# Optimization experiments

Hardware: AMD Instinct MI355X
Metric: run time of the kernel (lower is better)

Reference implementation:

```python
import jax, jax.numpy as jnp
import numpy as np

B, T, D, H = 2, 2048, 1024, 16
DH = D // H
EPS = 1e-5


def layer_norm(x, g, b):
    m = jnp.mean(x, axis=-1, keepdims=True)
    v = jnp.mean((x - m) ** 2, axis=-1, keepdims=True)
    return (x - m) * jax.lax.rsqrt(v + EPS) * g + b


def setup_inputs() -> dict:
    key = jax.random.key(0)
    ks = jax.random.split(key, 12)
    s = 0.02
    return {
        "x_refined": jax.random.normal(ks[0], (B, T, D), jnp.float32),
        "x_mem": jax.random.normal(ks[1], (B, T, D), jnp.float32),
        "ln_q_g": jnp.ones((D,), jnp.float32), "ln_q_b": jnp.zeros((D,), jnp.float32),
        "ln_kv_g": jnp.ones((D,), jnp.float32), "ln_kv_b": jnp.zeros((D,), jnp.float32),
        "Wq": jax.random.normal(ks[2], (D, D), jnp.float32) * s,
        "bq": jnp.zeros((D,), jnp.float32),
        "Wk": jax.random.normal(ks[3], (D, D), jnp.float32) * s,
        "bk": jnp.zeros((D,), jnp.float32),
        "Wv": jax.random.normal(ks[4], (D, D), jnp.float32) * s,
        "bv": jnp.zeros((D,), jnp.float32),
        "Wo": jax.random.normal(ks[5], (D, D), jnp.float32) * s,
        "bo": jnp.zeros((D,), jnp.float32),
        "ln_f_g": jnp.ones((D,), jnp.float32), "ln_f_b": jnp.zeros((D,), jnp.float32),
        "W1": jax.random.normal(ks[6], (D, 4 * D), jnp.float32) * s,
        "b1": jnp.zeros((4 * D,), jnp.float32),
        "W2": jax.random.normal(ks[7], (4 * D, D), jnp.float32) * s,
        "b2": jnp.zeros((D,), jnp.float32),
        "band": 24,
    }


def reference(x_refined, x_mem, ln_q_g, ln_q_b, ln_kv_g, ln_kv_b,
              Wq, bq, Wk, bk, Wv, bv, Wo, bo,
              ln_f_g, ln_f_b, W1, b1, W2, b2, band):
    Q = layer_norm(x_refined, ln_q_g, ln_q_b)   # (B,T,D)
    KV = layer_norm(x_mem, ln_kv_g, ln_kv_b)    # (B,T,D)

    # projections, split into heads: (B,H,T,DH)
    q = (Q @ Wq + bq).reshape(B, T, H, DH).transpose(0, 2, 1, 3)
    k = (KV @ Wk + bk).reshape(B, T, H, DH).transpose(0, 2, 1, 3)
    v = (KV @ Wv + bv).reshape(B, T, H, DH).transpose(0, 2, 1, 3)

    scores = jnp.einsum('bhtd,bhsd->bhts', q, k) / jnp.sqrt(jnp.float32(DH))
    # banded additive mask: |t - s| <= band allowed (same math as the Python loop)
    idx = jnp.arange(T)
    allowed = jnp.abs(idx[:, None] - idx[None, :]) <= band  # (T,T)
    scores = jnp.where(allowed[None, None], scores, -jnp.inf)
    attn = jax.nn.softmax(scores, axis=-1)

    ctx = jnp.einsum('bhts,bhsd->bhtd', attn, v)            # (B,H,T,DH)
    ctx = ctx.transpose(0, 2, 1, 3).reshape(B, T, D)
    y = x_refined + (ctx @ Wo + bo)

    h = layer_norm(y, ln_f_g, ln_f_b)
    h = jax.nn.gelu(h @ W1 + b1, approximate=False) @ W2 + b2
    return y + h
```

## Files before the change

kernel.cpp:

```cpp
#include <hip/hip_runtime.h>
#include <math.h>
#include <stdint.h>

#define TSEQ   2048
#define DMODEL 1024
#define NHEAD  16
#define DHEAD  64
#define MROWS  4096

typedef short bf16x8 __attribute__((ext_vector_type(8)));
typedef float f32x4  __attribute__((ext_vector_type(4)));
typedef uint64_t u64x2 __attribute__((ext_vector_type(2)));
typedef unsigned short u16;

typedef __attribute__((address_space(3))) unsigned int lds_u32_t;
typedef __attribute__((address_space(1))) unsigned int glb_u32_t;

static __device__ __forceinline__ u16 f2bf(float f) {
    unsigned u = __float_as_uint(f);
    u += 0x7FFFu + ((u >> 16) & 1u);
    return (u16)(u >> 16);
}
static __device__ __forceinline__ float bf2f(u16 h) {
    return __uint_as_float(((unsigned)h) << 16);
}

__global__ __launch_bounds__(256) void tc_kernel(
    const float* __restrict__ W, u16* __restrict__ Wt, int K, int N)
{
    __shared__ u16 tile[32][33];
    const int n0 = blockIdx.x * 32, k0 = blockIdx.y * 32;
    const int t = threadIdx.x;
    const int tx = t & 31, ty = t >> 5;
#pragma unroll
    for (int i = 0; i < 4; ++i) {
        int kk = ty + i * 8;
        tile[kk][tx] = f2bf(W[(size_t)(k0 + kk) * N + n0 + tx]);
    }
    __syncthreads();
#pragma unroll
    for (int i = 0; i < 4; ++i) {
        int nn = ty + i * 8;
        Wt[(size_t)(n0 + nn) * K + k0 + tx] = tile[tx][nn];
    }
}

__global__ __launch_bounds__(256) void biaspack_kernel(
    const float* __restrict__ bq, const float* __restrict__ bk,
    const float* __restrict__ bv, float* __restrict__ o)
{
    const int i = blockIdx.x * 256 + threadIdx.x;
    if (i < 1024) o[i] = bq[i];
    else if (i < 2048) o[i] = bk[i - 1024];
    else if (i < 3072) o[i] = bv[i - 2048];
}

__global__ __launch_bounds__(256) void vt_kernel(
    const u16* __restrict__ qkv, u16* __restrict__ vT)
{
    __shared__ __align__(16) u16 tile[64][72];
    const int bb = blockIdx.z;
    const int t0 = blockIdx.x * 64;
    const int c0 = blockIdx.y * 64;
    const int tid = threadIdx.x;
    const int r = tid >> 2;
    const int c = (tid & 3) * 16;
    const u16* src = qkv + (size_t)(bb * TSEQ + t0 + r) * 3072 + 2048 + c0 + c;
    *(bf16x8*)&tile[r][c]     = *(const bf16x8*)(src);
    *(bf16x8*)&tile[r][c + 8] = *(const bf16x8*)(src + 8);
    __syncthreads();
    u16 o[16];
#pragma unroll
    for (int j = 0; j < 16; ++j) o[j] = tile[c + j][r];
    u16* dst = vT + (size_t)(bb * 1024 + c0 + r) * TSEQ + t0 + c;
    *(bf16x8*)dst       = *(bf16x8*)&o[0];
    *(bf16x8*)(dst + 8) = *(bf16x8*)&o[8];
}

__global__ __launch_bounds__(256) void ln_kernel(
    const float* __restrict__ x, const float* __restrict__ g,
    const float* __restrict__ b, u16* __restrict__ out)
{
    const int row = blockIdx.x;
    const int t = threadIdx.x;
    const float4 v = ((const float4*)(x + (size_t)row * DMODEL))[t];
    float s  = v.x + v.y + v.z + v.w;
    float s2 = v.x * v.x + v.y * v.y + v.z * v.z + v.w * v.w;
#pragma unroll
    for (int m = 32; m >= 1; m >>= 1) { s += __shfl_xor(s, m); s2 += __shfl_xor(s2, m); }
    __shared__ float ps[4], ps2[4];
    if ((t & 63) == 0) { ps[t >> 6] = s; ps2[t >> 6] = s2; }
    __syncthreads();
    const float S  = ps[0] + ps[1] + ps[2] + ps[3];
    const float S2 = ps2[0] + ps2[1] + ps2[2] + ps2[3];
    const float mean = S * (1.0f / DMODEL);
    const float var  = S2 * (1.0f / DMODEL) - mean * mean;
    const float rstd = rsqrtf(var + 1e-5f);
    const float4 gg = ((const float4*)g)[t];
    const float4 bb = ((const float4*)b)[t];
    u16 o[4];
    o[0] = f2bf((v.x - mean) * rstd * gg.x + bb.x);
    o[1] = f2bf((v.y - mean) * rstd * gg.y + bb.y);
    o[2] = f2bf((v.z - mean) * rstd * gg.z + bb.z);
    o[3] = f2bf((v.w - mean) * rstd * gg.w + bb.w);
    *(short4*)(out + (size_t)row * DMODEL + t * 4) = *(short4*)o;
}

template <int EPI>
__global__ __launch_bounds__(512, 2) void gemm8(
    const u16* __restrict__ A, const u16* __restrict__ A2,
    const u16* __restrict__ Wt, const float* __restrict__ bias,
    u16* __restrict__ Cb, int N, int K, int gx, int cx)
{
    __shared__ __align__(16) char smem8[131072];

    const int bid = blockIdx.x;
    const int xcd = bid & 7, jj = bid >> 3;
    const int sx = gx / cx;
    const int sy = (gridDim.x >> 3) / sx;
    const int xr = xcd / cx, xc = xcd % cx;
    const int jr = jj / sx, jc = jj % sx;
    const int m0 = (xr * sy + jr) * 256;
    const int n0 = (xc * sx + jc) * 256;

    const int tid = threadIdx.x;
    const int lane = tid & 63;
    const int w = tid >> 6;
    const int wr = w >> 2, wc = w & 3;
    const int fr = lane & 15, fq = lane >> 4;
    const int swzoff = (fq ^ ((fr >> 1) & 3)) * 16;

    const u16* Ause = (A2 != nullptr && n0 >= 1024) ? A2 : A;

    const int strow = tid >> 2;
    const int stcol = ((tid & 3) ^ ((tid >> 3) & 3)) * 8;
    const u16* gAs = Ause + (size_t)(m0 + strow) * K + stcol;
    const u16* gBs = Wt  + (size_t)(n0 + strow) * K + stcol;

#define STAGE_A(slot, kt) do {                                                           \
    const u16* _s = gAs + (size_t)(kt) * 32;                                             \
    char* _l = smem8 + (slot) * 32768 + w * 1024;                                        \
    __builtin_amdgcn_global_load_lds((const glb_u32_t*)_s, (lds_u32_t*)_l, 16, 0, 0);    \
    __builtin_amdgcn_global_load_lds((const glb_u32_t*)(_s + (size_t)128 * K),           \
                                     (lds_u32_t*)(_l + 8192), 16, 0, 0);                 \
} while (0)
#define STAGE_B(slot, kt) do {                                                           \
    const u16* _s = gBs + (size_t)(kt) * 32;                                             \
    char* _l = smem8 + (slot) * 32768 + 16384 + w * 1024;                                \
    __builtin_amdgcn_global_load_lds((const glb_u32_t*)_s, (lds_u32_t*)_l, 16, 0, 0);    \
    __builtin_amdgcn_global_load_lds((const glb_u32_t*)(_s + (size_t)128 * K),           \
                                     (lds_u32_t*)(_l + 8192), 16, 0, 0);                 \
} while (0)

    f32x4 zero = {0.f, 0.f, 0.f, 0.f};
    f32x4 acc[8][4];
#pragma unroll
    for (int mi = 0; mi < 8; ++mi)
#pragma unroll
        for (int ni = 0; ni < 4; ++ni) acc[mi][ni] = zero;

    const int nt = K >> 5;
    STAGE_A(0, 0); STAGE_B(0, 0);
    STAGE_A(1, 1); STAGE_B(1, 1);

    const int abase = (wr * 128 + fr) * 64 + swzoff;
    const int bbase = 16384 + (wc * 64 + fr) * 64 + swzoff;

    for (int t = 0; t < nt; ++t) {
        const int slot = t & 3;
        const char* sb = smem8 + slot * 32768;
        asm volatile("s_waitcnt vmcnt(4)" ::: "memory");
        __builtin_amdgcn_s_barrier();

        bf16x8 bfr[4], af[4];
#pragma unroll
        for (int ni = 0; ni < 4; ++ni)
            bfr[ni] = *(const bf16x8*)(sb + bbase + ni * 1024);
#pragma unroll
        for (int mi = 0; mi < 4; ++mi)
            af[mi] = *(const bf16x8*)(sb + abase + mi * 1024);
        if (t + 2 < nt) STAGE_A((t + 2) & 3, t + 2);
        __builtin_amdgcn_s_setprio(1);
#pragma unroll
        for (int mi = 0; mi < 4; ++mi)
#pragma unroll
            for (int ni = 0; ni < 4; ++ni)
                acc[mi][ni] = __builtin_amdgcn_mfma_f32_16x16x32_bf16(af[mi], bfr[ni], acc[mi][ni], 0, 0, 0);
        __builtin_amdgcn_s_setprio(0);

        bf16x8 af2[4];
#pragma unroll
        for (int mi = 0; mi < 4; ++mi)
            af2[mi] = *(const bf16x8*)(sb + abase + (mi + 4) * 1024);
        if (t + 2 < nt) STAGE_B((t + 2) & 3, t + 2);
        __builtin_amdgcn_s_setprio(1);
#pragma unroll
        for (int mi = 0; mi < 4; ++mi)
#pragma unroll
            for (int ni = 0; ni < 4; ++ni)
                acc[mi + 4][ni] = __builtin_amdgcn_mfma_f32_16x16x32_bf16(af2[mi], bfr[ni], acc[mi + 4][ni], 0, 0, 0);
        __builtin_amdgcn_s_setprio(0);
    }
#undef STAGE_A
#undef STAGE_B

    u16* cs = (u16*)smem8;
#pragma unroll
    for (int hh = 0; hh < 2; ++hh) {
        __builtin_amdgcn_s_barrier();
        if (wr == hh) {
#pragma unroll
            for (int ni = 0; ni < 4; ++ni) {
                const int col = wc * 64 + ni * 16 + fr;
                const float bv = bias[n0 + col];
#pragma unroll
                for (int mi = 0; mi < 8; ++mi) {
#pragma unroll
                    for (int j = 0; j < 4; ++j) {
                        float val = acc[mi][ni][j] + bv;
                        if (EPI == 1)
                            val = 0.5f * val * (1.0f + erff(val * 0.70710678118654752f));
                        cs[(mi * 16 + fq * 4 + j) * 260 + col] = f2bf(val);
                    }
                }
            }
        }
        __builtin_amdgcn_s_barrier();
        const int cc = (tid & 31) * 8;
#pragma unroll
        for (int p = 0; p < 8; ++p) {
            const int row = p * 16 + (tid >> 5);
            const uint64_t lo = *(const uint64_t*)&cs[row * 260 + cc];
            const uint64_t hi = *(const uint64_t*)&cs[row * 260 + cc + 4];
            u64x2 v; v.x = lo; v.y = hi;
            *(u64x2*)&Cb[(size_t)(m0 + hh * 128 + row) * N + n0 + cc] = v;
        }
    }
}

template <int EPI>
__global__ __launch_bounds__(256) void gemm_bt(
    const u16* __restrict__ A, const u16* __restrict__ A2,
    const u16* __restrict__ Wt,
    const float* __restrict__ bias, const float* __restrict__ resid,
    u16* __restrict__ Cb, float* __restrict__ Cf, float* __restrict__ Cf2,
    int N, int K, int kl, int gx, int cx)
{
    extern __shared__ __align__(16) char smem[];

    const int bid = blockIdx.x;
    const int xcd = bid & 7, jj = bid >> 3;
    const int sx = gx / cx;
    const int sy = (gridDim.x >> 3) / sx;
    const int xr = xcd / cx, xc = xcd % cx;
    const int jr = jj / sx, jc = jj % sx;
    const int m0 = (xr * sy + jr) * 128;
    const int n0 = (xc * sx + jc) * 128;
    const int kofs = blockIdx.y * kl;

    const int t = threadIdx.x;
    const int lane = t & 63;
    const int wv = t >> 6;
    const int wr = wv >> 1, wc = wv & 1;

    const u16* Ause = (A2 != nullptr && n0 >= 1024) ? A2 : A;

    const int strow = t >> 2;
    const int stcol = (t & 3) * 8;
    const u16* gA  = Ause + (size_t)(m0 + strow) * K + kofs + stcol;
    const u16* gA2 = gA + (size_t)64 * K;
    const u16* gB  = Wt + (size_t)(n0 + strow) * K + kofs + stcol;
    const u16* gB2 = gB + (size_t)64 * K;

#define STAGE(bufi, k0) do {                                                            \
    char* _b = smem + (bufi) * 16384 + wv * 1024;                                       \
    __builtin_amdgcn_global_load_lds((const glb_u32_t*)(gA  + (k0)), (lds_u32_t*)(_b),          16, 0, 0); \
    __builtin_amdgcn_global_load_lds((const glb_u32_t*)(gA2 + (k0)), (lds_u32_t*)(_b + 4096),  16, 0, 0); \
    __builtin_amdgcn_global_load_lds((const glb_u32_t*)(gB  + (k0)), (lds_u32_t*)(_b + 8192),  16, 0, 0); \
    __builtin_amdgcn_global_load_lds((const glb_u32_t*)(gB2 + (k0)), (lds_u32_t*)(_b + 12288), 16, 0, 0); \
} while (0)

    f32x4 zero = {0.f, 0.f, 0.f, 0.f};
    f32x4 acc[4][4];
#pragma unroll
    for (int mi = 0; mi < 4; ++mi)
#pragma unroll
        for (int ni = 0; ni < 4; ++ni) acc[mi][ni] = zero;

    const int fr = lane & 15, fq = lane >> 4;
    const int nk = kl >> 5;

    STAGE(0, 0);
    STAGE(1, 32);

    for (int kt = 0; kt < nk; ++kt) {
        const int cur = kt & 1;
        if (kt < nk - 1) { asm volatile("s_waitcnt vmcnt(4)" ::: "memory"); }
        else             { asm volatile("s_waitcnt vmcnt(0)" ::: "memory"); }
        __builtin_amdgcn_s_barrier();

        const u16* As_ = (const u16*)smem + cur * 8192;
        const u16* Bs_ = As_ + 4096;
        bf16x8 af[4], bfr[4];
#pragma unroll
        for (int mi = 0; mi < 4; ++mi)
            af[mi] = *(const bf16x8*)&As_[(wr * 64 + mi * 16 + fr) * 32 + fq * 8];
#pragma unroll
        for (int ni = 0; ni < 4; ++ni)
            bfr[ni] = *(const bf16x8*)&Bs_[(wc * 64 + ni * 16 + fr) * 32 + fq * 8];

        __builtin_amdgcn_s_setprio(1);
#pragma unroll
        for (int mi = 0; mi < 4; ++mi)
#pragma unroll
            for (int ni = 0; ni < 4; ++ni)
                acc[mi][ni] = __builtin_amdgcn_mfma_f32_16x16x32_bf16(af[mi], bfr[ni], acc[mi][ni], 0, 0, 0);
        __builtin_amdgcn_s_setprio(0);
        __builtin_amdgcn_sched_barrier(0);
        __builtin_amdgcn_s_barrier();
        if (kt + 2 < nk) STAGE(cur, (kt + 2) << 5);
    }
#undef STAGE

    float* Cpart = (EPI == 3) ? (blockIdx.y ? Cf2 : Cf) : Cf;
#pragma unroll
    for (int ni = 0; ni < 4; ++ni) {
        const int col = n0 + wc * 64 + ni * 16 + fr;
        const float bv = (EPI == 3) ? 0.f : bias[col];
#pragma unroll
        for (int mi = 0; mi < 4; ++mi) {
#pragma unroll
            for (int j = 0; j < 4; ++j) {
                const int row = m0 + wr * 64 + mi * 16 + fq * 4 + j;
                float val = acc[mi][ni][j] + bv;
                if (EPI == 2)
                    Cf[(size_t)row * N + col] = val + resid[(size_t)row * N + col];
                else
                    Cpart[(size_t)row * N + col] = val;
            }
        }
    }
}

__global__ __launch_bounds__(256) void redk_kernel(
    const float* __restrict__ p0, const float* __restrict__ p1,
    const float* __restrict__ bias, const float* __restrict__ resid,
    float* __restrict__ out, int n4, int ncols)
{
    const int stride = gridDim.x * 256;
    for (int i = blockIdx.x * 256 + threadIdx.x; i < n4; i += stride) {
        const float4 a = ((const float4*)p0)[i];
        const float4 b = ((const float4*)p1)[i];
        const float4 r = ((const float4*)resid)[i];
        const float4 bb = *(const float4*)&bias[(i * 4) & (ncols - 1)];
        float4 o;
        o.x = a.x + b.x + bb.x + r.x;
        o.y = a.y + b.y + bb.y + r.y;
        o.z = a.z + b.z + bb.z + r.z;
        o.w = a.w + b.w + bb.w + r.w;
        ((float4*)out)[i] = o;
    }
}

__global__ __launch_bounds__(256) void battn_kernel(
    const u16* __restrict__ qkv, const u16* __restrict__ vT,
    u16* __restrict__ ctx, const int* __restrict__ band_ptr)
{
    __shared__ __align__(16) u16 P[4][16][104];
    const int band = *band_ptr;
    const int bid = blockIdx.x;
    const int tile = bid & 31;
    const int h = (bid >> 5) & 15;
    const int b = bid >> 9;
    const int w = threadIdx.x >> 6;
    const int lane = threadIdx.x & 63;
    const int fr = lane & 15, fq = lane >> 4;
    const int t0 = tile * 64 + w * 16;

    const size_t qbase = ((size_t)b * TSEQ) * 3072 + h * DHEAD;
    const size_t kbase = qbase + 1024;
    const size_t cbase = ((size_t)b * TSEQ) * DMODEL + h * DHEAD;

    const bf16x8 aq0 = *(const bf16x8*)&qkv[qbase + (size_t)(t0 + fr) * 3072 + fq * 8];
    const bf16x8 aq1 = *(const bf16x8*)&qkv[qbase + (size_t)(t0 + fr) * 3072 + 32 + fq * 8];

    const int kb0 = t0 - 32;
    const f32x4 zero = {0.f, 0.f, 0.f, 0.f};

    f32x4 sc[5];
#pragma unroll
    for (int kt = 0; kt < 5; ++kt) {
        const int srow = kb0 + kt * 16 + fr;
        const int scl = min(max(srow, 0), TSEQ - 1);
        const bf16x8 kf0 = *(const bf16x8*)&qkv[kbase + (size_t)scl * 3072 + fq * 8];
        const bf16x8 kf1 = *(const bf16x8*)&qkv[kbase + (size_t)scl * 3072 + 32 + fq * 8];
        f32x4 a = zero;
        a = __builtin_amdgcn_mfma_f32_16x16x32_bf16(aq0, kf0, a, 0, 0, 0);
        a = __builtin_amdgcn_mfma_f32_16x16x32_bf16(aq1, kf1, a, 0, 0, 0);
        sc[kt] = a;
    }

    float mx[4], l[4];
#pragma unroll
    for (int j = 0; j < 4; ++j) mx[j] = -1e30f;
#pragma unroll
    for (int kt = 0; kt < 5; ++kt) {
        const int s = kb0 + kt * 16 + fr;
#pragma unroll
        for (int j = 0; j < 4; ++j) {
            const int tq = t0 + fq * 4 + j;
            const bool ok = (s >= 0) && (s < TSEQ) && (abs(tq - s) <= band);
            const float vv = ok ? sc[kt][j] * 0.125f : -1e30f;
            sc[kt][j] = vv;
            mx[j] = fmaxf(mx[j], vv);
        }
    }
#pragma unroll
    for (int m = 1; m <= 8; m <<= 1)
#pragma unroll
        for (int j = 0; j < 4; ++j) mx[j] = fmaxf(mx[j], __shfl_xor(mx[j], m));

#pragma unroll
    for (int j = 0; j < 4; ++j) l[j] = 0.f;
#pragma unroll
    for (int kt = 0; kt < 5; ++kt)
#pragma unroll
        for (int j = 0; j < 4; ++j) {
            const float p = __expf(sc[kt][j] - mx[j]);
            sc[kt][j] = p;
            l[j] += p;
        }
#pragma unroll
    for (int m = 1; m <= 8; m <<= 1)
#pragma unroll
        for (int j = 0; j < 4; ++j) l[j] += __shfl_xor(l[j], m);

#pragma unroll
    for (int kt = 0; kt < 5; ++kt)
#pragma unroll
        for (int j = 0; j < 4; ++j)
            P[w][fq * 4 + j][kt * 16 + fr] = f2bf(sc[kt][j]);
    {
        const short4 z4 = {0, 0, 0, 0};
        *(short4*)&P[w][fr][80 + fq * 4] = z4;
    }
    __syncthreads();

    bf16x8 pa[3];
#pragma unroll
    for (int c = 0; c < 3; ++c)
        pa[c] = *(const bf16x8*)&P[w][fr][c * 32 + fq * 8];

    const size_t vbase = ((size_t)(b * NHEAD + h) * DHEAD) * TSEQ;
    f32x4 cacc[4];
#pragma unroll
    for (int dt = 0; dt < 4; ++dt) cacc[dt] = zero;
#pragma unroll
    for (int dt = 0; dt < 4; ++dt) {
#pragma unroll
        for (int c = 0; c < 3; ++c) {
            const int s8 = kb0 + c * 32 + fq * 8;
            const int s8c = min(max(s8, 0), TSEQ - 8);
            const bf16x8 vf = *(const bf16x8*)&vT[vbase + (size_t)(dt * 16 + fr) * TSEQ + s8c];
            cacc[dt] = __builtin_amdgcn_mfma_f32_16x16x32_bf16(pa[c], vf, cacc[dt], 0, 0, 0);
        }
    }

    float rl[4];
#pragma unroll
    for (int j = 0; j < 4; ++j) rl[j] = 1.0f / l[j];
#pragma unroll
    for (int dt = 0; dt < 4; ++dt)
#pragma unroll
        for (int j = 0; j < 4; ++j)
            ctx[cbase + (size_t)(t0 + fq * 4 + j) * DMODEL + dt * 16 + fr] =
                f2bf(cacc[dt][j] * rl[j]);
}

extern "C" void kernel_launch(void* const* d_in, const int* in_sizes, int n_in,
                              void* d_out, int out_size, void* d_ws, size_t ws_size,
                              hipStream_t stream) {
    const float* x_ref  = (const float*)d_in[0];
    const float* x_mem  = (const float*)d_in[1];
    const float* ln_q_g = (const float*)d_in[2];
    const float* ln_q_b = (const float*)d_in[3];
    const float* ln_kv_g= (const float*)d_in[4];
    const float* ln_kv_b= (const float*)d_in[5];
    const float* Wq = (const float*)d_in[6];
    const float* bq = (const float*)d_in[7];
    const float* Wk = (const float*)d_in[8];
    const float* bk = (const float*)d_in[9];
    const float* Wv = (const float*)d_in[10];
    const float* bv = (const float*)d_in[11];
    const float* Wo = (const float*)d_in[12];
    const float* bo = (const float*)d_in[13];
    const float* ln_f_g = (const float*)d_in[14];
    const float* ln_f_b = (const float*)d_in[15];
    const float* W1 = (const float*)d_in[16];
    const float* b1 = (const float*)d_in[17];
    const float* W2 = (const float*)d_in[18];
    const float* b2 = (const float*)d_in[19];
    const int*  band = (const int*)d_in[20];
    float* out = (float*)d_out;

    char* ws = (char*)d_ws;
    const size_t MB = 1024 * 1024;
    if (ws_size < 128 * MB) return;
    u16*   wt_qkv = (u16*)(ws + 0 * MB);
    u16*   wt_o   = (u16*)(ws + 6 * MB);
    u16*   wt_1   = (u16*)(ws + 8 * MB);
    u16*   wt_2   = (u16*)(ws + 16 * MB);
    float* bqkv   = (float*)(ws + 24 * MB);
    u16*   aq     = (u16*)(ws + 25 * MB);
    u16*   akv    = (u16*)(ws + 33 * MB);
    u16*   qkvb   = (u16*)(ws + 41 * MB);
    u16*   vTb    = (u16*)(ws + 65 * MB);
    u16*   ctxb   = (u16*)(ws + 73 * MB);
    float* y      = (float*)(ws + 81 * MB);
    u16*   hb     = (u16*)(ws + 97 * MB);
    u16*   a1     = (u16*)(ws + 25 * MB);
    float* p0     = (float*)(ws + 57 * MB);
    float* p1     = (float*)(ws + 97 * MB);

    dim3 blk(256);
    const size_t SM_GEMM = 32768;

    tc_kernel<<<dim3(32, 32),  blk, 0, stream>>>(Wq, wt_qkv,               1024, 1024);
    tc_kernel<<<dim3(32, 32),  blk, 0, stream>>>(Wk, wt_qkv + 1024 * 1024, 1024, 1024);
    tc_kernel<<<dim3(32, 32),  blk, 0, stream>>>(Wv, wt_qkv + 2048 * 1024, 1024, 1024);
    tc_kernel<<<dim3(32, 32),  blk, 0, stream>>>(Wo, wt_o, 1024, 1024);
    tc_kernel<<<dim3(128, 32), blk, 0, stream>>>(W1, wt_1, 1024, 4096);
    tc_kernel<<<dim3(32, 128), blk, 0, stream>>>(W2, wt_2, 4096, 1024);
    biaspack_kernel<<<12, blk, 0, stream>>>(bq, bk, bv, bqkv);
    ln_kernel<<<MROWS, blk, 0, stream>>>(x_ref, ln_q_g, ln_q_b, aq);
    ln_kernel<<<MROWS, blk, 0, stream>>>(x_mem, ln_kv_g, ln_kv_b, akv);
    gemm8<0><<<dim3(192), dim3(512), 0, stream>>>(aq, akv, wt_qkv, bqkv, qkvb,
                                                  3072, 1024, 12, 2);
    vt_kernel<<<dim3(32, 16, 2), blk, 0, stream>>>(qkvb, vTb);
    battn_kernel<<<1024, blk, 0, stream>>>(qkvb, vTb, ctxb, band);
    gemm_bt<2><<<dim3(256), blk, SM_GEMM, stream>>>(ctxb, nullptr, wt_o, bo, x_ref,
                                                    nullptr, y, nullptr,
                                                    1024, 1024, 1024, 8, 1);
    ln_kernel<<<MROWS, blk, 0, stream>>>(y, ln_f_g, ln_f_b, hb);
    gemm8<1><<<dim3(256), dim3(512), 0, stream>>>(hb, nullptr, wt_1, b1, a1,
                                                  4096, 1024, 16, 2);
    gemm_bt<3><<<dim3(256, 2), blk, SM_GEMM, stream>>>(a1, nullptr, wt_2, nullptr, nullptr,
                                                       nullptr, p0, p1,
                                                       1024, 4096, 2048, 8, 1);
    redk_kernel<<<2048, blk, 0, stream>>>(p0, p1, b2, y, out, MROWS * 1024 / 4, 1024);
}
```

Measured before the change: 384.8 us.

## Restructure 256x256 GEMM main loop into K=64 double-buffered, eight-phase ping-pong schedule

Rewrites the main loop of the 256x256 bf16 GEMM used for the QKV and FFN-up projections. Each K tile is now 64 wide instead of 32, with two 64 KB LDS buffers and an 8-way XOR swizzle. Each tile is split into four quarter-phases, each issuing one global-to-LDS load chunk, followed by barriers and a block of MFMAs. The aim is finer interleaving of loads and matrix math and fewer loop iterations per K element. The cost is many more barriers per iteration and a hand-tuned vmcnt schedule that could stall or be fragile.

Result: no change. 382.8 us (-0.5%).

```diff
diff --git a/kernel.cpp b/kernel.cpp
--- a/kernel.cpp
+++ b/kernel.cpp
@@ -106,8 +106,10 @@
     *(short4*)(out + (size_t)row * DMODEL + t * 4) = *(short4*)o;
 }
 
+#define MFMA16 __builtin_amdgcn_mfma_f32_16x16x32_bf16
+
 template <int EPI>
-__global__ __launch_bounds__(512, 2) void gemm8(
+__global__ __launch_bounds__(512, 2) void gemm256(
     const u16* __restrict__ A, const u16* __restrict__ A2,
     const u16* __restrict__ Wt, const float* __restrict__ bias,
     u16* __restrict__ Cb, int N, int K, int gx, int cx)
@@ -128,81 +130,211 @@
     const int w = tid >> 6;
     const int wr = w >> 2, wc = w & 3;
     const int fr = lane & 15, fq = lane >> 4;
-    const int swzoff = (fq ^ ((fr >> 1) & 3)) * 16;
+    const int s0 = (fq ^ (fr & 7)) * 16;
 
     const u16* Ause = (A2 != nullptr && n0 >= 1024) ? A2 : A;
 
-    const int strow = tid >> 2;
-    const int stcol = ((tid & 3) ^ ((tid >> 3) & 3)) * 8;
-    const u16* gAs = Ause + (size_t)(m0 + strow) * K + stcol;
-    const u16* gBs = Wt  + (size_t)(n0 + strow) * K + stcol;
-
-#define STAGE_A(slot, kt) do {                                                           \
-    const u16* _s = gAs + (size_t)(kt) * 32;                                             \
-    char* _l = smem8 + (slot) * 32768 + w * 1024;                                        \
-    __builtin_amdgcn_global_load_lds((const glb_u32_t*)_s, (lds_u32_t*)_l, 16, 0, 0);    \
-    __builtin_amdgcn_global_load_lds((const glb_u32_t*)(_s + (size_t)128 * K),           \
+    const int strow = tid >> 3;
+    const int stcol = ((tid & 7) ^ ((tid >> 3) & 7)) * 8;
+    const u16* gA0 = Ause + (size_t)(m0 + strow) * K + stcol;
+    const u16* gA1 = gA0 + (size_t)128 * K;
+    const u16* gB0 = Wt + (size_t)(n0 + strow) * K + stcol;
+    const u16* gB1 = gB0 + (size_t)128 * K;
+    const size_t jstep = (size_t)64 * K;
+
+#define SH(ldsoff, gp, kt) do {                                                          \
+    char* _l = smem8 + (ldsoff) + w * 1024;                                              \
+    const u16* _g = (gp) + (size_t)(kt) * 64;                                            \
+    __builtin_amdgcn_global_load_lds((const glb_u32_t*)_g, (lds_u32_t*)_l, 16, 0, 0);    \
+    __builtin_amdgcn_global_load_lds((const glb_u32_t*)(_g + jstep),                     \
                                      (lds_u32_t*)(_l + 8192), 16, 0, 0);                 \
 } while (0)
-#define STAGE_B(slot, kt) do {                                                           \
-    const u16* _s = gBs + (size_t)(kt) * 32;                                             \
-    char* _l = smem8 + (slot) * 32768 + 16384 + w * 1024;                                \
-    __builtin_amdgcn_global_load_lds((const glb_u32_t*)_s, (lds_u32_t*)_l, 16, 0, 0);    \
-    __builtin_amdgcn_global_load_lds((const glb_u32_t*)(_s + (size_t)128 * K),           \
-                                     (lds_u32_t*)(_l + 8192), 16, 0, 0);                 \
-} while (0)
-
-    f32x4 zero = {0.f, 0.f, 0.f, 0.f};
+
     f32x4 acc[8][4];
 #pragma unroll
-    for (int mi = 0; mi < 8; ++mi)
-#pragma unroll
-        for (int ni = 0; ni < 4; ++ni) acc[mi][ni] = zero;
-
-    const int nt = K >> 5;
-    STAGE_A(0, 0); STAGE_B(0, 0);
-    STAGE_A(1, 1); STAGE_B(1, 1);
-
-    const int abase = (wr * 128 + fr) * 64 + swzoff;
-    const int bbase = 16384 + (wc * 64 + fr) * 64 + swzoff;
-
-    for (int t = 0; t < nt; ++t) {
-        const int slot = t & 3;
-        const char* sb = smem8 + slot * 32768;
-        asm volatile("s_waitcnt vmcnt(4)" ::: "memory");
-        __builtin_amdgcn_s_barrier();
-
-        bf16x8 bfr[4], af[4];
-#pragma unroll
-        for (int ni = 0; ni < 4; ++ni)
-            bfr[ni] = *(const bf16x8*)(sb + bbase + ni * 1024);
-#pragma unroll
-        for (int mi = 0; mi < 4; ++mi)
-            af[mi] = *(const bf16x8*)(sb + abase + mi * 1024);
-        if (t + 2 < nt) STAGE_A((t + 2) & 3, t + 2);
-        __builtin_amdgcn_s_setprio(1);
-#pragma unroll
-        for (int mi = 0; mi < 4; ++mi)
-#pragma unroll
-            for (int ni = 0; ni < 4; ++ni)
-                acc[mi][ni] = __builtin_amdgcn_mfma_f32_16x16x32_bf16(af[mi], bfr[ni], acc[mi][ni], 0, 0, 0);
-        __builtin_amdgcn_s_setprio(0);
-
-        bf16x8 af2[4];
-#pragma unroll
-        for (int mi = 0; mi < 4; ++mi)
-            af2[mi] = *(const bf16x8*)(sb + abase + (mi + 4) * 1024);
-        if (t + 2 < nt) STAGE_B((t + 2) & 3, t + 2);
-        __builtin_amdgcn_s_setprio(1);
-#pragma unroll
-        for (int mi = 0; mi < 4; ++mi)
-#pragma unroll
-            for (int ni = 0; ni < 4; ++ni)
-                acc[mi + 4][ni] = __builtin_amdgcn_mfma_f32_16x16x32_bf16(af2[mi], bfr[ni], acc[mi + 4][ni], 0, 0, 0);
-        __builtin_amdgcn_s_setprio(0);
-    }
-#undef STAGE_A
-#undef STAGE_B
+    for (int m = 0; m < 8; ++m)
+#pragma unroll
+        for (int n = 0; n < 4; ++n) acc[m][n] = (f32x4){0.f, 0.f, 0.f, 0.f};
+
+    const int aob = wr * 16384 + fr * 128 + s0;
+    const int bob = 32768 + (wc >> 1) * 16384 + ((wc & 1) * 64 + fr) * 128 + s0;
+
+    const int nt = K >> 6;
+    const int niter = nt >> 1;
+
+    SH(0,     gA0, 0); SH(16384, gA1, 0); SH(32768, gB0, 0); SH(49152, gB1, 0);
+    SH(65536, gA0, 1);
+    asm volatile("s_waitcnt vmcnt(6)" ::: "memory");
+    __builtin_amdgcn_s_barrier();
+
+    bf16x8 af[4][2], bfr[4][2];
+
+    for (int i = 0; i < niter; ++i) {
+        const bool more = (i + 1 < niter);
+        const int kt1 = 2 * i + 1, kt2 = kt1 + 1, kt3 = kt1 + 2;
+        const char* sb0 = smem8;
+        const char* sb1 = smem8 + 65536;
+
+#pragma unroll
+        for (int m = 0; m < 4; ++m) {
+            const int o = aob + m * 2048;
+            af[m][0] = *(const bf16x8*)(sb0 + o);
+            af[m][1] = *(const bf16x8*)(sb0 + (o ^ 64));
+        }
+#pragma unroll
+        for (int n = 0; n < 2; ++n) {
+            const int o = bob + n * 2048;
+            bfr[n][0] = *(const bf16x8*)(sb0 + o);
+            bfr[n][1] = *(const bf16x8*)(sb0 + (o ^ 64));
+        }
+        SH(65536 + 16384, gA1, kt1);
+        __builtin_amdgcn_s_barrier();
+        asm volatile("s_waitcnt lgkmcnt(0)" ::: "memory");
+        __builtin_amdgcn_s_setprio(1);
+#pragma unroll
+        for (int m = 0; m < 4; ++m)
+#pragma unroll
+            for (int n = 0; n < 2; ++n) {
+                acc[m][n] = MFMA16(af[m][0], bfr[n][0], acc[m][n], 0, 0, 0);
+                acc[m][n] = MFMA16(af[m][1], bfr[n][1], acc[m][n], 0, 0, 0);
+            }
+        __builtin_amdgcn_s_setprio(0);
+        __builtin_amdgcn_s_barrier();
+
+#pragma unroll
+        for (int n = 2; n < 4; ++n) {
+            const int o = bob + n * 2048;
+            bfr[n][0] = *(const bf16x8*)(sb0 + o);
+            bfr[n][1] = *(const bf16x8*)(sb0 + (o ^ 64));
+        }
+        SH(65536 + 32768, gB0, kt1);
+        __builtin_amdgcn_s_barrier();
+        asm volatile("s_waitcnt lgkmcnt(0)" ::: "memory");
+        __builtin_amdgcn_s_setprio(1);
+#pragma unroll
+        for (int m = 0; m < 4; ++m)
+#pragma unroll
+            for (int n = 2; n < 4; ++n) {
+                acc[m][n] = MFMA16(af[m][0], bfr[n][0], acc[m][n], 0, 0, 0);
+                acc[m][n] = MFMA16(af[m][1], bfr[n][1], acc[m][n], 0, 0, 0);
+            }
+        __builtin_amdgcn_s_setprio(0);
+        __builtin_amdgcn_s_barrier();
+
+#pragma unroll
+        for (int m = 0; m < 4; ++m) {
+            const int o = aob + 8192 + m * 2048;
+            af[m][0] = *(const bf16x8*)(sb0 + o);
+            af[m][1] = *(const bf16x8*)(sb0 + (o ^ 64));
+        }
+        SH(65536 + 49152, gB1, kt1);
+        __builtin_amdgcn_s_barrier();
+        asm volatile("s_waitcnt lgkmcnt(0)" ::: "memory");
+        __builtin_amdgcn_s_setprio(1);
+#pragma unroll
+        for (int m = 0; m < 4; ++m)
+#pragma unroll
+            for (int n = 0; n < 2; ++n) {
+                acc[m + 4][n] = MFMA16(af[m][0], bfr[n][0], acc[m + 4][n], 0, 0, 0);
+                acc[m + 4][n] = MFMA16(af[m][1], bfr[n][1], acc[m + 4][n], 0, 0, 0);
+            }
+        __builtin_amdgcn_s_setprio(0);
+        __builtin_amdgcn_s_barrier();
+
+        if (more) { SH(0, gA0, kt2); asm volatile("s_waitcnt vmcnt(6)" ::: "memory"); }
+        else      {                  asm volatile("s_waitcnt vmcnt(0)" ::: "memory"); }
+        __builtin_amdgcn_s_barrier();
+        __builtin_amdgcn_s_setprio(1);
+#pragma unroll
+        for (int m = 0; m < 4; ++m)
+#pragma unroll
+            for (int n = 2; n < 4; ++n) {
+                acc[m + 4][n] = MFMA16(af[m][0], bfr[n][0], acc[m + 4][n], 0, 0, 0);
+                acc[m + 4][n] = MFMA16(af[m][1], bfr[n][1], acc[m + 4][n], 0, 0, 0);
+            }
+        __builtin_amdgcn_s_setprio(0);
+        __builtin_amdgcn_s_barrier();
+
+#pragma unroll
+        for (int m = 0; m < 4; ++m) {
+            const int o = aob + m * 2048;
+            af[m][0] = *(const bf16x8*)(sb1 + o);
+            af[m][1] = *(const bf16x8*)(sb1 + (o ^ 64));
+        }
+#pragma unroll
+        for (int n = 0; n < 2; ++n) {
+            const int o = bob + n * 2048;
+            bfr[n][0] = *(const bf16x8*)(sb1 + o);
+            bfr[n][1] = *(const bf16x8*)(sb1 + (o ^ 64));
+        }
+        if (more) SH(16384, gA1, kt2);
+        __builtin_amdgcn_s_barrier();
+        asm volatile("s_waitcnt lgkmcnt(0)" ::: "memory");
+        __builtin_amdgcn_s_setprio(1);
+#pragma unroll
+        for (int m = 0; m < 4; ++m)
+#pragma unroll
+            for (int n = 0; n < 2; ++n) {
+                acc[m][n] = MFMA16(af[m][0], bfr[n][0], acc[m][n], 0, 0, 0);
+                acc[m][n] = MFMA16(af[m][1], bfr[n][1], acc[m][n], 0, 0, 0);
+            }
+        __builtin_amdgcn_s_setprio(0);
+        __builtin_amdgcn_s_barrier();
+
+#pragma unroll
+        for (int n = 2; n < 4; ++n) {
+            const int o = bob + n * 2048;
+            bfr[n][0] = *(const bf16x8*)(sb1 + o);
+            bfr[n][1] = *(const bf16x8*)(sb1 + (o ^ 64));
+        }
+        if (more) SH(32768, gB0, kt2);
+        __builtin_amdgcn_s_barrier();
+        asm volatile("s_waitcnt lgkmcnt(0)" ::: "memory");
+        __builtin_amdgcn_s_setprio(1);
+#pragma unroll
+        for (int m = 0; m < 4; ++m)
+#pragma unroll
+            for (int n = 2; n < 4; ++n) {
+                acc[m][n] = MFMA16(af[m][0], bfr[n][0], acc[m][n], 0, 0, 0);
+                acc[m][n] = MFMA16(af[m][1], bfr[n][1], acc[m][n], 0, 0, 0);
+            }
+        __builtin_amdgcn_s_setprio(0);
+        __builtin_amdgcn_s_barrier();
+
+#pragma unroll
+        for (int m = 0; m < 4; ++m) {
+            const int o = aob + 8192 + m * 2048;
+            af[m][0] = *(const bf16x8*)(sb1 + o);
+            af[m][1] = *(const bf16x8*)(sb1 + (o ^ 64));
+        }
+        if (more) SH(49152, gB1, kt2);
+        __builtin_amdgcn_s_barrier();
+        asm volatile("s_waitcnt lgkmcnt(0)" ::: "memory");
+        __builtin_amdgcn_s_setprio(1);
+#pragma unroll
+        for (int m = 0; m < 4; ++m)
+#pragma unroll
+            for (int n = 0; n < 2; ++n) {
+                acc[m + 4][n] = MFMA16(af[m][0], bfr[n][0], acc[m + 4][n], 0, 0, 0);
+                acc[m + 4][n] = MFMA16(af[m][1], bfr[n][1], acc[m + 4][n], 0, 0, 0);
+            }
+        __builtin_amdgcn_s_setprio(0);
+        __builtin_amdgcn_s_barrier();
+
+        if (more) { SH(65536, gA0, kt3); asm volatile("s_waitcnt vmcnt(6)" ::: "memory"); }
+        __builtin_amdgcn_s_barrier();
+        __builtin_amdgcn_s_setprio(1);
+#pragma unroll
+        for (int m = 0; m < 4; ++m)
+#pragma unroll
+            for (int n = 2; n < 4; ++n) {
+                acc[m + 4][n] = MFMA16(af[m][0], bfr[n][0], acc[m + 4][n], 0, 0, 0);
+                acc[m + 4][n] = MFMA16(af[m][1], bfr[n][1], acc[m + 4][n], 0, 0, 0);
+            }
+        __builtin_amdgcn_s_setprio(0);
+        __builtin_amdgcn_s_barrier();
+    }
+#undef SH
 
     u16* cs = (u16*)smem8;
 #pragma unroll
@@ -314,7 +446,7 @@
         for (int mi = 0; mi < 4; ++mi)
 #pragma unroll
             for (int ni = 0; ni < 4; ++ni)
-                acc[mi][ni] = __builtin_amdgcn_mfma_f32_16x16x32_bf16(af[mi], bfr[ni], acc[mi][ni], 0, 0, 0);
+                acc[mi][ni] = MFMA16(af[mi], bfr[ni], acc[mi][ni], 0, 0, 0);
         __builtin_amdgcn_s_setprio(0);
         __builtin_amdgcn_sched_barrier(0);
         __builtin_amdgcn_s_barrier();
@@ -395,8 +527,8 @@
         const bf16x8 kf0 = *(const bf16x8*)&qkv[kbase + (size_t)scl * 3072 + fq * 8];
         const bf16x8 kf1 = *(const bf16x8*)&qkv[kbase + (size_t)scl * 3072 + 32 + fq * 8];
         f32x4 a = zero;
-        a = __builtin_amdgcn_mfma_f32_16x16x32_bf16(aq0, kf0, a, 0, 0, 0);
-        a = __builtin_amdgcn_mfma_f32_16x16x32_bf16(aq1, kf1, a, 0, 0, 0);
+        a = MFMA16(aq0, kf0, a, 0, 0, 0);
+        a = MFMA16(aq1, kf1, a, 0, 0, 0);
         sc[kt] = a;
     }
 
@@ -462,7 +594,7 @@
             const int s8 = kb0 + c * 32 + fq * 8;
             const int s8c = min(max(s8, 0), TSEQ - 8);
             const bf16x8 vf = *(const bf16x8*)&vT[vbase + (size_t)(dt * 16 + fr) * TSEQ + s8c];
-            cacc[dt] = __builtin_amdgcn_mfma_f32_16x16x32_bf16(pa[c], vf, cacc[dt], 0, 0, 0);
+            cacc[dt] = MFMA16(pa[c], vf, cacc[dt], 0, 0, 0);
         }
     }
 
@@ -534,16 +666,16 @@
     biaspack_kernel<<<12, blk, 0, stream>>>(bq, bk, bv, bqkv);
     ln_kernel<<<MROWS, blk, 0, stream>>>(x_ref, ln_q_g, ln_q_b, aq);
     ln_kernel<<<MROWS, blk, 0, stream>>>(x_mem, ln_kv_g, ln_kv_b, akv);
-    gemm8<0><<<dim3(192), dim3(512), 0, stream>>>(aq, akv, wt_qkv, bqkv, qkvb,
-                                                  3072, 1024, 12, 2);
+    gemm256<0><<<dim3(192), dim3(512), 0, stream>>>(aq, akv, wt_qkv, bqkv, qkvb,
+                                                    3072, 1024, 12, 2);
     vt_kernel<<<dim3(32, 16, 2), blk, 0, stream>>>(qkvb, vTb);
     battn_kernel<<<1024, blk, 0, stream>>>(qkvb, vTb, ctxb, band);
     gemm_bt<2><<<dim3(256), blk, SM_GEMM, stream>>>(ctxb, nullptr, wt_o, bo, x_ref,
                                                     nullptr, y, nullptr,
                                                     1024, 1024, 1024, 8, 1);
     ln_kernel<<<MROWS, blk, 0, stream>>>(y, ln_f_g, ln_f_b, hb);
-    gemm8<1><<<dim3(256), dim3(512), 0, stream>>>(hb, nullptr, wt_1, b1, a1,
-                                                  4096, 1024, 16, 2);
+    gemm256<1><<<dim3(256), dim3(512), 0, stream>>>(hb, nullptr, wt_1, b1, a1,
+                                                    4096, 1024, 16, 2);
     gemm_bt<3><<<dim3(256, 2), blk, SM_GEMM, stream>>>(a1, nullptr, wt_2, nullptr, nullptr,
                                                        nullptr, p0, p1,
                                                        1024, 4096, 2048, 8, 1);
```
